# Performance work log

Measured on AMD Instinct MI355X. Metric: run time of the kernel, lower is better.

## Reference

```python
import jax, jax.numpy as jnp
import numpy as np

EPS = 1e-8


def setup_inputs() -> dict:
    key = jax.random.key(0)
    k1, k2, k3 = jax.random.split(key, 3)
    K_, M, N = 2048, 512, 64
    x = jax.random.normal(k1, (K_, M), dtype=jnp.float32)
    w_att = jax.random.uniform(k2, (M, M), dtype=jnp.float32)
    w_b = jax.random.uniform(k3, (M, N), dtype=jnp.float32)
    return {"x": x, "w_att": w_att, "w_b": w_b, "l": 8}


def reference(x, w_att, w_b, l):
    # soft attention scores over features: [k, m]
    scores_soft = jax.nn.softmax(x @ w_att, axis=-1) + EPS
    # per-target l-th largest value of w_b over the m axis -> threshold [n]
    thr = jax.lax.top_k(w_b.T, l)[0][:, -1]  # [n]
    sh = w_b - thr[None, :] + EPS  # [m, n]
    # training-phase soft hard-mask: clamp to [-1, 1], shift to [0, 1]
    scores_hard = (jnp.clip(sh, -1.0, 1.0) + 1.0) * 0.5  # [m, n]
    # outer-product combine: 'mn,km->kmn' then 'kmn,km->kmn'
    mask_weight = scores_hard[None, :, :] * scores_soft[:, :, None]  # [k, m, n]
    out = mask_weight * x[:, :, None]  # [k, m, n]
    return out, scores_hard, scores_soft, mask_weight
```

## Files before the change

kernel.cpp:

```cpp
#include <hip/hip_runtime.h>
#include <math.h>

#define K_DIM 2048
#define M_DIM 512
#define N_DIM 64
#define EPSF 1e-8f
#define ROWS 8
#define TPB 512

typedef float f32x4 __attribute__((ext_vector_type(4)));

__global__ __launch_bounds__(256) void thr_hard_kernel(
    const float* __restrict__ w_b, const int* __restrict__ lptr,
    float* __restrict__ scores_hard) {
  __shared__ float col[M_DIM];
  __shared__ float red[256];
  const int n = blockIdx.x;
  const int t = threadIdx.x;
  const int L = lptr[0];

  col[t]       = w_b[t * N_DIM + n];
  col[t + 256] = w_b[(t + 256) * N_DIM + n];
  __syncthreads();

  const float v0 = col[t], v1 = col[t + 256];
  int c0 = 0, c1 = 0;
  for (int i = 0; i < M_DIM; ++i) {
    const float c = col[i];
    c0 += (c > v0);
    c1 += (c > v1);
  }
  float cand0 = (c0 <= L - 1) ? v0 : INFINITY;
  float cand1 = (c1 <= L - 1) ? v1 : INFINITY;
  red[t] = fminf(cand0, cand1);
  __syncthreads();
  for (int s = 128; s > 0; s >>= 1) {
    if (t < s) red[t] = fminf(red[t], red[t + s]);
    __syncthreads();
  }
  const float thr = red[0];

  {
    float sh0 = (col[t] - thr) + EPSF;
    float sh1 = (col[t + 256] - thr) + EPSF;
    sh0 = fminf(fmaxf(sh0, -1.0f), 1.0f);
    sh1 = fminf(fmaxf(sh1, -1.0f), 1.0f);
    scores_hard[t * N_DIM + n]         = (sh0 + 1.0f) * 0.5f;
    scores_hard[(t + 256) * N_DIM + n] = (sh1 + 1.0f) * 0.5f;
  }
}

__global__ __launch_bounds__(TPB) void fused_kernel(
    const float* __restrict__ x, const float* __restrict__ w,
    const float* __restrict__ hard, float* __restrict__ soft,
    f32x4* __restrict__ out, f32x4* __restrict__ mw) {
  __shared__ float xs[ROWS][M_DIM];
  __shared__ float sm[ROWS][M_DIM];
  const int t = threadIdx.x;
  const int k0 = blockIdx.x * ROWS;

  {
    const f32x4* xg = (const f32x4*)(x + (size_t)k0 * M_DIM);
    f32x4* xsv = (f32x4*)&xs[0][0];
    xsv[t]       = xg[t];
    xsv[t + TPB] = xg[t + TPB];
  }
  __syncthreads();

  float acc[ROWS];
#pragma unroll
  for (int r = 0; r < ROWS; ++r) acc[r] = 0.0f;

#pragma unroll 2
  for (int m = 0; m < M_DIM; m += 4) {
    const float w0 = w[(m + 0) * M_DIM + t];
    const float w1 = w[(m + 1) * M_DIM + t];
    const float w2 = w[(m + 2) * M_DIM + t];
    const float w3 = w[(m + 3) * M_DIM + t];
#pragma unroll
    for (int r = 0; r < ROWS; ++r) {
      const float4 xv = *(const float4*)&xs[r][m];
      acc[r] += xv.x * w0 + xv.y * w1 + xv.z * w2 + xv.w * w3;
    }
  }
#pragma unroll
  for (int r = 0; r < ROWS; ++r) sm[r][t] = acc[r];
  __syncthreads();

  {
    const int r = t >> 6, ln = t & 63;
    float v[8];
    float mx = -INFINITY;
#pragma unroll
    for (int i = 0; i < 8; ++i) {
      v[i] = sm[r][ln + 64 * i];
      mx = fmaxf(mx, v[i]);
    }
#pragma unroll
    for (int s = 32; s > 0; s >>= 1) mx = fmaxf(mx, __shfl_xor(mx, s));
    float sum = 0.0f;
#pragma unroll
    for (int i = 0; i < 8; ++i) {
      v[i] = expf(v[i] - mx);
      sum += v[i];
    }
#pragma unroll
    for (int s = 32; s > 0; s >>= 1) sum += __shfl_xor(sum, s);
    const float inv = 1.0f / sum;
#pragma unroll
    for (int i = 0; i < 8; ++i) sm[r][ln + 64 * i] = v[i] * inv + EPSF;
  }
  __syncthreads();

  {
    const f32x4* smv = (const f32x4*)&sm[0][0];
    f32x4* sg = (f32x4*)(soft + (size_t)k0 * M_DIM);
    __builtin_nontemporal_store(smv[t], &sg[t]);
    __builtin_nontemporal_store(smv[t + TPB], &sg[t + TPB]);
  }

  const f32x4* hard4 = (const f32x4*)hard;
  const size_t base = (size_t)k0 * (M_DIM * (N_DIM / 4));
#pragma unroll 4
  for (int it = 0; it < (ROWS * M_DIM * 16) / TPB; ++it) {
    const int g = it * TPB + t;
    const int q = g & 15;
    const int pair = g >> 4;
    const int m = pair & (M_DIM - 1);
    const int r = pair >> 9;
    const float ss = sm[r][m];
    const float xv = xs[r][m];
    const f32x4 sh = hard4[m * 16 + q];
    const f32x4 wgt = sh * ss;
    const f32x4 o = wgt * xv;
    __builtin_nontemporal_store(o, &out[base + g]);
    __builtin_nontemporal_store(wgt, &mw[base + g]);
  }
}

extern "C" void kernel_launch(void* const* d_in, const int* in_sizes, int n_in,
                              void* d_out, int out_size, void* d_ws,
                              size_t ws_size, hipStream_t stream) {
  const float* x     = (const float*)d_in[0];
  const float* w_att = (const float*)d_in[1];
  const float* w_b   = (const float*)d_in[2];
  const int*   lptr  = (const int*)d_in[3];

  float* out_base = (float*)d_out;
  const size_t OUT_SZ = (size_t)K_DIM * M_DIM * N_DIM;
  float* out0 = out_base;
  float* hard = out0 + OUT_SZ;
  float* soft = hard + (size_t)M_DIM * N_DIM;
  float* mwp  = soft + (size_t)K_DIM * M_DIM;

  thr_hard_kernel<<<N_DIM, 256, 0, stream>>>(w_b, lptr, hard);
  fused_kernel<<<K_DIM / ROWS, TPB, 0, stream>>>(
      x, w_att, hard, soft, (f32x4*)out0, (f32x4*)mwp);
}
```

Baseline: 615.6 us.

## Retile matmul to 4 rows x 2 columns per thread and use plain stores

Each thread in the x@w_att stage now computes a 4-row by 2-column tile instead of one column across 8 rows. Every thread therefore loads 8 weight values per step rather than 4, and each LDS read of x feeds twice as many FMAs. The large output writes and the soft-score writes switch from nontemporal stores to ordinary stores. Ordinary stores change how the 256MB of output moves through the cache and could help or hurt write bandwidth, which dominates runtime.

Measured after the change: 578.3 us. -6.0%, faster.

```diff
diff --git a/kernel.cpp b/kernel.cpp
--- a/kernel.cpp
+++ b/kernel.cpp
@@ -67,24 +67,35 @@
   }
   __syncthreads();
 
-  float acc[ROWS];
+  {
+    const int half = t >> 8;
+    const int j0 = t & 255;
+    const int r0 = half * 4;
+    float acc[4][2];
 #pragma unroll
-  for (int r = 0; r < ROWS; ++r) acc[r] = 0.0f;
+    for (int r = 0; r < 4; ++r) { acc[r][0] = 0.0f; acc[r][1] = 0.0f; }
 
 #pragma unroll 2
-  for (int m = 0; m < M_DIM; m += 4) {
-    const float w0 = w[(m + 0) * M_DIM + t];
-    const float w1 = w[(m + 1) * M_DIM + t];
-    const float w2 = w[(m + 2) * M_DIM + t];
-    const float w3 = w[(m + 3) * M_DIM + t];
+    for (int m = 0; m < M_DIM; m += 4) {
+      float wa[4], wb[4];
 #pragma unroll
-    for (int r = 0; r < ROWS; ++r) {
-      const float4 xv = *(const float4*)&xs[r][m];
-      acc[r] += xv.x * w0 + xv.y * w1 + xv.z * w2 + xv.w * w3;
+      for (int i = 0; i < 4; ++i) {
+        wa[i] = w[(m + i) * M_DIM + j0];
+        wb[i] = w[(m + i) * M_DIM + j0 + 256];
+      }
+#pragma unroll
+      for (int r = 0; r < 4; ++r) {
+        const float4 xv = *(const float4*)&xs[r0 + r][m];
+        acc[r][0] += xv.x * wa[0] + xv.y * wa[1] + xv.z * wa[2] + xv.w * wa[3];
+        acc[r][1] += xv.x * wb[0] + xv.y * wb[1] + xv.z * wb[2] + xv.w * wb[3];
+      }
+    }
+#pragma unroll
+    for (int r = 0; r < 4; ++r) {
+      sm[r0 + r][j0]       = acc[r][0];
+      sm[r0 + r][j0 + 256] = acc[r][1];
     }
   }
-#pragma unroll
-  for (int r = 0; r < ROWS; ++r) sm[r][t] = acc[r];
   __syncthreads();
 
   {
@@ -115,8 +126,8 @@
   {
     const f32x4* smv = (const f32x4*)&sm[0][0];
     f32x4* sg = (f32x4*)(soft + (size_t)k0 * M_DIM);
-    __builtin_nontemporal_store(smv[t], &sg[t]);
-    __builtin_nontemporal_store(smv[t + TPB], &sg[t + TPB]);
+    sg[t]       = smv[t];
+    sg[t + TPB] = smv[t + TPB];
   }
 
   const f32x4* hard4 = (const f32x4*)hard;
@@ -133,8 +144,8 @@
     const f32x4 sh = hard4[m * 16 + q];
     const f32x4 wgt = sh * ss;
     const f32x4 o = wgt * xv;
-    __builtin_nontemporal_store(o, &out[base + g]);
-    __builtin_nontemporal_store(wgt, &mw[base + g]);
+    out[base + g] = o;
+    mw[base + g]  = wgt;
   }
 }
 
```

## Retile matmul to vector columns and split output stores into separate streams

Applied to the files above, without the earlier changes.

The x@w_att stage now has each thread compute four adjacent columns for two rows using float4 loads of w, in place of one column for all eight rows. The outer-product writes are split into two loops, one for out and one for mask_weight, so each loop streams to a single destination. Nontemporal stores are replaced with regular stores. The product is reordered to sh*(ss*xv), which changes float rounding slightly, and w_att is now read four times per block since each row pair reloads the full matrix.

Result: faster. 596.3 us (-3.1%).

```diff
diff --git a/kernel.cpp b/kernel.cpp
--- a/kernel.cpp
+++ b/kernel.cpp
@@ -67,24 +67,28 @@
   }
   __syncthreads();
 
-  float acc[ROWS];
-#pragma unroll
-  for (int r = 0; r < ROWS; ++r) acc[r] = 0.0f;
+  {
+    const int grp = t >> 7;
+    const int c = t & 127;
+    const int j0 = c * 4;
+    const int r0 = grp * 2;
+    f32x4 acc0 = {0.f, 0.f, 0.f, 0.f};
+    f32x4 acc1 = {0.f, 0.f, 0.f, 0.f};
 
 #pragma unroll 2
-  for (int m = 0; m < M_DIM; m += 4) {
-    const float w0 = w[(m + 0) * M_DIM + t];
-    const float w1 = w[(m + 1) * M_DIM + t];
-    const float w2 = w[(m + 2) * M_DIM + t];
-    const float w3 = w[(m + 3) * M_DIM + t];
-#pragma unroll
-    for (int r = 0; r < ROWS; ++r) {
-      const float4 xv = *(const float4*)&xs[r][m];
-      acc[r] += xv.x * w0 + xv.y * w1 + xv.z * w2 + xv.w * w3;
+    for (int m = 0; m < M_DIM; m += 4) {
+      f32x4 wv0 = *(const f32x4*)&w[(m + 0) * M_DIM + j0];
+      f32x4 wv1 = *(const f32x4*)&w[(m + 1) * M_DIM + j0];
+      f32x4 wv2 = *(const f32x4*)&w[(m + 2) * M_DIM + j0];
+      f32x4 wv3 = *(const f32x4*)&w[(m + 3) * M_DIM + j0];
+      const float4 xa = *(const float4*)&xs[r0 + 0][m];
+      const float4 xb = *(const float4*)&xs[r0 + 1][m];
+      acc0 += wv0 * xa.x + wv1 * xa.y + wv2 * xa.z + wv3 * xa.w;
+      acc1 += wv0 * xb.x + wv1 * xb.y + wv2 * xb.z + wv3 * xb.w;
     }
+    *(f32x4*)&sm[r0 + 0][j0] = acc0;
+    *(f32x4*)&sm[r0 + 1][j0] = acc1;
   }
-#pragma unroll
-  for (int r = 0; r < ROWS; ++r) sm[r][t] = acc[r];
   __syncthreads();
 
   {
@@ -115,26 +119,35 @@
   {
     const f32x4* smv = (const f32x4*)&sm[0][0];
     f32x4* sg = (f32x4*)(soft + (size_t)k0 * M_DIM);
-    __builtin_nontemporal_store(smv[t], &sg[t]);
-    __builtin_nontemporal_store(smv[t + TPB], &sg[t + TPB]);
+    sg[t]       = smv[t];
+    sg[t + TPB] = smv[t + TPB];
   }
 
   const f32x4* hard4 = (const f32x4*)hard;
   const size_t base = (size_t)k0 * (M_DIM * (N_DIM / 4));
-#pragma unroll 4
+#pragma unroll 8
   for (int it = 0; it < (ROWS * M_DIM * 16) / TPB; ++it) {
     const int g = it * TPB + t;
     const int q = g & 15;
-    const int pair = g >> 4;
-    const int m = pair & (M_DIM - 1);
-    const int r = pair >> 9;
+    const int pm = g >> 4;
+    const int m = pm & (M_DIM - 1);
+    const int r = pm >> 9;
     const float ss = sm[r][m];
     const float xv = xs[r][m];
     const f32x4 sh = hard4[m * 16 + q];
-    const f32x4 wgt = sh * ss;
-    const f32x4 o = wgt * xv;
-    __builtin_nontemporal_store(o, &out[base + g]);
-    __builtin_nontemporal_store(wgt, &mw[base + g]);
+    out[base + g] = sh * (ss * xv);
+  }
+
+#pragma unroll 8
+  for (int it = 0; it < (ROWS * M_DIM * 16) / TPB; ++it) {
+    const int g = it * TPB + t;
+    const int q = g & 15;
+    const int pm = g >> 4;
+    const int m = pm & (M_DIM - 1);
+    const int r = pm >> 9;
+    const float ss = sm[r][m];
+    const f32x4 sh = hard4[m * 16 + q];
+    mw[base + g] = sh * ss;
   }
 }
 
```
